# Kernel tuning notes

Hardware: AMD Instinct MI355X
Metric: run time of the kernel (lower is better)

Reference implementation:

```python
import jax, jax.numpy as jnp
import numpy as np

N_NODES = 100000

def setup_inputs() -> dict:
    key = jax.random.key(0)
    k1, k2, k3, k4, k5, k6 = jax.random.split(key, 6)
    input = jax.random.normal(k1, (N_NODES, 256), dtype=jnp.float32)
    weight = jax.random.normal(k2, (256, 256), dtype=jnp.float32) * (1.0 / np.sqrt(256))
    bias = jax.random.normal(k3, (256,), dtype=jnp.float32) * 0.02
    edge_rows = jax.random.randint(k4, (3200000,), 0, N_NODES, dtype=jnp.int32)
    edge_cols = jax.random.randint(k5, (3200000,), 0, N_NODES, dtype=jnp.int32)
    edge_vals = jax.random.uniform(k6, (3200000,), dtype=jnp.float32)
    return {"input": input, "weight": weight, "bias": bias,
            "edge_rows": edge_rows, "edge_cols": edge_cols, "edge_vals": edge_vals}

def reference(input, weight, bias, edge_rows, edge_cols, edge_vals):
    # support = X @ W  -- dense GEMM [N, in] x [in, out]
    support = input @ weight
    # output = spmm(adj, support): out[r] += adj[r,c] * support[c]
    gathered = support[edge_cols] * edge_vals[:, None]          # [E, out]
    output = jax.ops.segment_sum(gathered, edge_rows, num_segments=N_NODES)
    return output + bias
```

## Files before the change

kernel.cpp:

```cpp
#include <hip/hip_runtime.h>
#include <hip/hip_bf16.h>
#include <stdint.h>

#define M_NODES 100000
#define DIM     256
#define N_EDGES 3200000
#define CAP     80
#define CHUNK   8192
#define NWG1    391
#define NB      391
#define BCAP    9216

typedef __bf16 bf16x8 __attribute__((ext_vector_type(8)));
typedef float  f32x4  __attribute__((ext_vector_type(4)));
typedef unsigned short u16x8 __attribute__((ext_vector_type(8)));

__device__ __forceinline__ unsigned short f2bf(float f) {
    unsigned u = __float_as_uint(f);
    u += 0x7FFF + ((u >> 16) & 1);
    return (unsigned short)(u >> 16);
}
__device__ __forceinline__ float bf2f(unsigned short h) {
    return __uint_as_float(((unsigned)h) << 16);
}

__global__ __launch_bounds__(256) void k_convert_wt(const float* __restrict__ W,
                                                    unsigned short* __restrict__ Wt,
                                                    int* __restrict__ cur) {
    int k = blockIdx.x, n = threadIdx.x;
    Wt[n * 256 + k] = f2bf(W[k * 256 + n]);
    int gid = k * 256 + n;
    if (gid < NB) cur[gid] = 0;
}

__global__ __launch_bounds__(256) void k_gemm(const float* __restrict__ X,
                                              const unsigned short* __restrict__ Wt,
                                              unsigned short* __restrict__ Sb) {
    int wave = threadIdx.x >> 6;
    int lane = threadIdx.x & 63;
    int tile = blockIdx.x * 4 + wave;
    if (tile >= M_NODES / 16) return;
    int m0   = tile * 16;
    int quad = lane >> 4;
    int r    = lane & 15;

    const float* aptr = X + (size_t)(m0 + r) * 256 + quad * 8;

    f32x4 acc[16];
#pragma unroll
    for (int t = 0; t < 16; ++t) acc[t] = {0.f, 0.f, 0.f, 0.f};

#pragma unroll
    for (int k0 = 0; k0 < 256; k0 += 32) {
        f32x4 a0 = *(const f32x4*)(aptr + k0);
        f32x4 a1 = *(const f32x4*)(aptr + k0 + 4);
        unsigned short au[8];
        au[0] = f2bf(a0.x); au[1] = f2bf(a0.y); au[2] = f2bf(a0.z); au[3] = f2bf(a0.w);
        au[4] = f2bf(a1.x); au[5] = f2bf(a1.y); au[6] = f2bf(a1.z); au[7] = f2bf(a1.w);
        bf16x8 a = *(bf16x8*)au;
#pragma unroll
        for (int t = 0; t < 16; ++t) {
            bf16x8 b = *(const bf16x8*)(Wt + (size_t)(t * 16 + r) * 256 + k0 + quad * 8);
            acc[t] = __builtin_amdgcn_mfma_f32_16x16x32_bf16(a, b, acc[t], 0, 0, 0);
        }
    }

#pragma unroll
    for (int t = 0; t < 16; ++t)
#pragma unroll
        for (int i = 0; i < 4; ++i)
            Sb[(size_t)(m0 + quad * 4 + i) * 256 + t * 16 + r] = f2bf(acc[t][i]);
}

__global__ __launch_bounds__(512) void k_part2(const int* __restrict__ rows,
                                               const int* __restrict__ cols,
                                               const float* __restrict__ vals,
                                               uint64_t* __restrict__ part,
                                               int* __restrict__ cur) {
    __shared__ int cnt[NB];
    __shared__ int wcur[NB];
    int w = blockIdx.x, t = threadIdx.x;
    int base = w * CHUNK;
    int clen = N_EDGES - base; if (clen > CHUNK) clen = CHUNK;

    for (int i = t; i < NB; i += 512) cnt[i] = 0;
    __syncthreads();
    for (int i = t; i < clen; i += 512)
        atomicAdd(&cnt[rows[base + i] >> 8], 1);
    __syncthreads();

    for (int b = t; b < NB; b += 512)
        wcur[b] = atomicAdd(&cur[b], cnt[b]);
    __syncthreads();

    for (int i = t; i < clen; i += 512) {
        int   r = rows[base + i];
        int   c = cols[base + i];
        float v = vals[base + i];
        int   b = r >> 8;
        int pos = atomicAdd(&wcur[b], 1);
        if (pos < BCAP) {
            uint32_t lo = (uint32_t)c | ((uint32_t)(r & 255) << 17);
            part[(size_t)b * BCAP + pos] = ((uint64_t)__float_as_uint(v) << 32) | lo;
        }
    }
}

__global__ __launch_bounds__(512) void k_build3(const uint64_t* __restrict__ part,
                                                const int* __restrict__ cur,
                                                uint32_t* __restrict__ csr4,
                                                int* __restrict__ counts) {
    __shared__ int lcnt[256];
    int b = blockIdx.x, t = threadIdx.x;
    if (t < 256) lcnt[t] = 0;
    int n = cur[b];
    if (n > BCAP) n = BCAP;
    __syncthreads();

    const uint64_t* p = part + (size_t)b * BCAP;
    for (int i = t; i < n; i += 512) {
        uint64_t ent = p[i];
        uint32_t lo  = (uint32_t)ent;
        int   rl = (lo >> 17) & 255;
        int   c  = lo & 0x1FFFF;
        float v  = __uint_as_float((uint32_t)(ent >> 32));
        int qv = (int)(v * 32768.f + 0.5f);
        if (qv > 32767) qv = 32767;
        int pos = atomicAdd(&lcnt[rl], 1);
        if (pos < CAP)
            csr4[(size_t)(b * 256 + rl) * CAP + pos] = ((uint32_t)c << 15) | (uint32_t)qv;
    }
    __syncthreads();
    if (t < 256) counts[b * 256 + t] = lcnt[t];
}

__global__ __launch_bounds__(256) void k_spmm(const int* __restrict__ counts,
                                              const uint32_t* __restrict__ csr4,
                                              const unsigned short* __restrict__ Sb,
                                              const float* __restrict__ bias,
                                              float* __restrict__ out) {
    int wave = threadIdx.x >> 6;
    int lane = threadIdx.x & 63;
    int r = blockIdx.x * 4 + wave;
    if (r >= M_NODES) return;
    int n = counts[r];
    if (n > CAP) n = CAP;
    const uint32_t* ep = csr4 + (size_t)r * CAP;
    int half = lane >> 5;
    int l    = lane & 31;

    float acc[8] = {0.f, 0.f, 0.f, 0.f, 0.f, 0.f, 0.f, 0.f};
    int j = 0;
    for (; j + 7 < n; j += 8) {
        uint32_t m0 = ep[j +     half];
        uint32_t m1 = ep[j + 2 + half];
        uint32_t m2 = ep[j + 4 + half];
        uint32_t m3 = ep[j + 6 + half];
        int c0 = m0 >> 15;  float v0 = (float)(m0 & 0x7FFF) * (1.f / 32768.f);
        int c1 = m1 >> 15;  float v1 = (float)(m1 & 0x7FFF) * (1.f / 32768.f);
        int c2 = m2 >> 15;  float v2 = (float)(m2 & 0x7FFF) * (1.f / 32768.f);
        int c3 = m3 >> 15;  float v3 = (float)(m3 & 0x7FFF) * (1.f / 32768.f);
        u16x8 s0 = *(const u16x8*)(Sb + (size_t)c0 * 256 + l * 8);
        u16x8 s1 = *(const u16x8*)(Sb + (size_t)c1 * 256 + l * 8);
        u16x8 s2 = *(const u16x8*)(Sb + (size_t)c2 * 256 + l * 8);
        u16x8 s3 = *(const u16x8*)(Sb + (size_t)c3 * 256 + l * 8);
#pragma unroll
        for (int i = 0; i < 8; ++i) acc[i] += bf2f(s0[i]) * v0;
#pragma unroll
        for (int i = 0; i < 8; ++i) acc[i] += bf2f(s1[i]) * v1;
#pragma unroll
        for (int i = 0; i < 8; ++i) acc[i] += bf2f(s2[i]) * v2;
#pragma unroll
        for (int i = 0; i < 8; ++i) acc[i] += bf2f(s3[i]) * v3;
    }
    for (; j + 1 < n; j += 2) {
        uint32_t m0 = ep[j + half];
        int c0 = m0 >> 15;  float v0 = (float)(m0 & 0x7FFF) * (1.f / 32768.f);
        u16x8 s0 = *(const u16x8*)(Sb + (size_t)c0 * 256 + l * 8);
#pragma unroll
        for (int i = 0; i < 8; ++i) acc[i] += bf2f(s0[i]) * v0;
    }
    if (j < n && half == 0) {
        uint32_t m0 = ep[j];
        int c0 = m0 >> 15;  float v0 = (float)(m0 & 0x7FFF) * (1.f / 32768.f);
        u16x8 s0 = *(const u16x8*)(Sb + (size_t)c0 * 256 + l * 8);
#pragma unroll
        for (int i = 0; i < 8; ++i) acc[i] += bf2f(s0[i]) * v0;
    }

#pragma unroll
    for (int i = 0; i < 8; ++i) acc[i] += __shfl(acc[i], lane + 32);

    if (half == 0) {
        f32x4 b0 = *(const f32x4*)(bias + l * 8);
        f32x4 b1 = *(const f32x4*)(bias + l * 8 + 4);
        f32x4 o0 = {acc[0] + b0.x, acc[1] + b0.y, acc[2] + b0.z, acc[3] + b0.w};
        f32x4 o1 = {acc[4] + b1.x, acc[5] + b1.y, acc[6] + b1.z, acc[7] + b1.w};
        float* op = out + (size_t)r * 256 + l * 8;
        *(f32x4*)op       = o0;
        *(f32x4*)(op + 4) = o1;
    }
}

extern "C" void kernel_launch(void* const* d_in, const int* in_sizes, int n_in,
                              void* d_out, int out_size, void* d_ws, size_t ws_size,
                              hipStream_t stream) {
    const float* X    = (const float*)d_in[0];
    const float* W    = (const float*)d_in[1];
    const float* bias = (const float*)d_in[2];
    const int*   er   = (const int*)d_in[3];
    const int*   ec   = (const int*)d_in[4];
    const float* ev   = (const float*)d_in[5];
    float* out = (float*)d_out;

    char* ws = (char*)d_ws;
    unsigned short* Wt     = (unsigned short*)ws;
    uint32_t*       csr4   = (uint32_t*)(ws + 131072);
    int*            cur    = (int*)(ws + 32161792);
    int*            counts = (int*)(ws + 32166912);
    uint64_t*       part   = (uint64_t*)(ws + 32567296);
    unsigned short* Sb     = (unsigned short*)(ws + 32567296);

    k_convert_wt<<<256,   256, 0, stream>>>(W, Wt, cur);
    k_part2     <<<NWG1,  512, 0, stream>>>(er, ec, ev, part, cur);
    k_build3    <<<NB,    512, 0, stream>>>(part, cur, csr4, counts);
    k_gemm      <<<1563,  256, 0, stream>>>(X, Wt, Sb);
    k_spmm      <<<25000, 256, 0, stream>>>(counts, csr4, Sb, bias, out);
}
```

Measured before the change: 615.0 us.

## Fuse GEMM and edge partitioning into one kernel with interleaved block roles

The dense GEMM and the edge bucketing pass now run in a single launch: even blocks compute a GEMM tile and odd blocks partition a smaller edge chunk. This lets the compute-bound GEMM overlap with the memory- and atomic-bound partition step and drops one launch. Because the two now run at the same time, Sb moves to its own workspace region instead of aliasing part. The build kernel goes to 1024 threads per block, and empty buckets skip their global atomic. Smaller chunks mean more global atomics on the bucket cursors, and the mixed block roles may unbalance the workload.

```diff
diff --git a/kernel.cpp b/kernel.cpp
--- a/kernel.cpp
+++ b/kernel.cpp
@@ -6,8 +6,8 @@
 #define DIM     256
 #define N_EDGES 3200000
 #define CAP     80
-#define CHUNK   8192
-#define NWG1    391
+#define CHUNK   2048
+#define NCHUNK  1563
 #define NB      391
 #define BCAP    9216
 
@@ -33,67 +33,72 @@
     if (gid < NB) cur[gid] = 0;
 }
 
-__global__ __launch_bounds__(256) void k_gemm(const float* __restrict__ X,
-                                              const unsigned short* __restrict__ Wt,
-                                              unsigned short* __restrict__ Sb) {
-    int wave = threadIdx.x >> 6;
-    int lane = threadIdx.x & 63;
-    int tile = blockIdx.x * 4 + wave;
-    if (tile >= M_NODES / 16) return;
-    int m0   = tile * 16;
-    int quad = lane >> 4;
-    int r    = lane & 15;
-
-    const float* aptr = X + (size_t)(m0 + r) * 256 + quad * 8;
-
-    f32x4 acc[16];
-#pragma unroll
-    for (int t = 0; t < 16; ++t) acc[t] = {0.f, 0.f, 0.f, 0.f};
-
-#pragma unroll
-    for (int k0 = 0; k0 < 256; k0 += 32) {
-        f32x4 a0 = *(const f32x4*)(aptr + k0);
-        f32x4 a1 = *(const f32x4*)(aptr + k0 + 4);
-        unsigned short au[8];
-        au[0] = f2bf(a0.x); au[1] = f2bf(a0.y); au[2] = f2bf(a0.z); au[3] = f2bf(a0.w);
-        au[4] = f2bf(a1.x); au[5] = f2bf(a1.y); au[6] = f2bf(a1.z); au[7] = f2bf(a1.w);
-        bf16x8 a = *(bf16x8*)au;
-#pragma unroll
-        for (int t = 0; t < 16; ++t) {
-            bf16x8 b = *(const bf16x8*)(Wt + (size_t)(t * 16 + r) * 256 + k0 + quad * 8);
-            acc[t] = __builtin_amdgcn_mfma_f32_16x16x32_bf16(a, b, acc[t], 0, 0, 0);
-        }
-    }
-
-#pragma unroll
-    for (int t = 0; t < 16; ++t)
-#pragma unroll
-        for (int i = 0; i < 4; ++i)
-            Sb[(size_t)(m0 + quad * 4 + i) * 256 + t * 16 + r] = f2bf(acc[t][i]);
-}
-
-__global__ __launch_bounds__(512) void k_part2(const int* __restrict__ rows,
+__global__ __launch_bounds__(256) void k_fused(const float* __restrict__ X,
+                                               const unsigned short* __restrict__ Wt,
+                                               unsigned short* __restrict__ Sb,
+                                               const int* __restrict__ rows,
                                                const int* __restrict__ cols,
                                                const float* __restrict__ vals,
                                                uint64_t* __restrict__ part,
                                                int* __restrict__ cur) {
     __shared__ int cnt[NB];
     __shared__ int wcur[NB];
-    int w = blockIdx.x, t = threadIdx.x;
+    int bid = blockIdx.x;
+    int t   = threadIdx.x;
+
+    if ((bid & 1) == 0) {
+        int wave = t >> 6;
+        int lane = t & 63;
+        int tile = (bid >> 1) * 4 + wave;
+        if (tile >= M_NODES / 16) return;
+        int m0   = tile * 16;
+        int quad = lane >> 4;
+        int r    = lane & 15;
+
+        const float* aptr = X + (size_t)(m0 + r) * 256 + quad * 8;
+
+        f32x4 acc[16];
+#pragma unroll
+        for (int tt = 0; tt < 16; ++tt) acc[tt] = {0.f, 0.f, 0.f, 0.f};
+
+#pragma unroll
+        for (int k0 = 0; k0 < 256; k0 += 32) {
+            f32x4 a0 = *(const f32x4*)(aptr + k0);
+            f32x4 a1 = *(const f32x4*)(aptr + k0 + 4);
+            unsigned short au[8];
+            au[0] = f2bf(a0.x); au[1] = f2bf(a0.y); au[2] = f2bf(a0.z); au[3] = f2bf(a0.w);
+            au[4] = f2bf(a1.x); au[5] = f2bf(a1.y); au[6] = f2bf(a1.z); au[7] = f2bf(a1.w);
+            bf16x8 a = *(bf16x8*)au;
+#pragma unroll
+            for (int tt = 0; tt < 16; ++tt) {
+                bf16x8 b = *(const bf16x8*)(Wt + (size_t)(tt * 16 + r) * 256 + k0 + quad * 8);
+                acc[tt] = __builtin_amdgcn_mfma_f32_16x16x32_bf16(a, b, acc[tt], 0, 0, 0);
+            }
+        }
+
+#pragma unroll
+        for (int tt = 0; tt < 16; ++tt)
+#pragma unroll
+            for (int i = 0; i < 4; ++i)
+                Sb[(size_t)(m0 + quad * 4 + i) * 256 + tt * 16 + r] = f2bf(acc[tt][i]);
+        return;
+    }
+
+    int w    = bid >> 1;
     int base = w * CHUNK;
     int clen = N_EDGES - base; if (clen > CHUNK) clen = CHUNK;
 
-    for (int i = t; i < NB; i += 512) cnt[i] = 0;
-    __syncthreads();
-    for (int i = t; i < clen; i += 512)
+    for (int i = t; i < NB; i += 256) cnt[i] = 0;
+    __syncthreads();
+    for (int i = t; i < clen; i += 256)
         atomicAdd(&cnt[rows[base + i] >> 8], 1);
     __syncthreads();
 
-    for (int b = t; b < NB; b += 512)
-        wcur[b] = atomicAdd(&cur[b], cnt[b]);
-    __syncthreads();
-
-    for (int i = t; i < clen; i += 512) {
+    for (int b = t; b < NB; b += 256)
+        if (cnt[b]) wcur[b] = atomicAdd(&cur[b], cnt[b]);
+    __syncthreads();
+
+    for (int i = t; i < clen; i += 256) {
         int   r = rows[base + i];
         int   c = cols[base + i];
         float v = vals[base + i];
@@ -106,10 +111,10 @@
     }
 }
 
-__global__ __launch_bounds__(512) void k_build3(const uint64_t* __restrict__ part,
-                                                const int* __restrict__ cur,
-                                                uint32_t* __restrict__ csr4,
-                                                int* __restrict__ counts) {
+__global__ __launch_bounds__(1024) void k_build3(const uint64_t* __restrict__ part,
+                                                 const int* __restrict__ cur,
+                                                 uint32_t* __restrict__ csr4,
+                                                 int* __restrict__ counts) {
     __shared__ int lcnt[256];
     int b = blockIdx.x, t = threadIdx.x;
     if (t < 256) lcnt[t] = 0;
@@ -118,7 +123,7 @@
     __syncthreads();
 
     const uint64_t* p = part + (size_t)b * BCAP;
-    for (int i = t; i < n; i += 512) {
+    for (int i = t; i < n; i += 1024) {
         uint64_t ent = p[i];
         uint32_t lo  = (uint32_t)ent;
         int   rl = (lo >> 17) & 255;
@@ -219,11 +224,10 @@
     int*            cur    = (int*)(ws + 32161792);
     int*            counts = (int*)(ws + 32166912);
     uint64_t*       part   = (uint64_t*)(ws + 32567296);
-    unsigned short* Sb     = (unsigned short*)(ws + 32567296);
-
-    k_convert_wt<<<256,   256, 0, stream>>>(W, Wt, cur);
-    k_part2     <<<NWG1,  512, 0, stream>>>(er, ec, ev, part, cur);
-    k_build3    <<<NB,    512, 0, stream>>>(part, cur, csr4, counts);
-    k_gemm      <<<1563,  256, 0, stream>>>(X, Wt, Sb);
-    k_spmm      <<<25000, 256, 0, stream>>>(counts, csr4, Sb, bias, out);
-}
+    unsigned short* Sb     = (unsigned short*)(ws + 61394944);
+
+    k_convert_wt<<<256,        256,  0, stream>>>(W, Wt, cur);
+    k_fused     <<<2 * NCHUNK, 256,  0, stream>>>(X, Wt, Sb, er, ec, ev, part, cur);
+    k_build3    <<<NB,         1024, 0, stream>>>(part, cur, csr4, counts);
+    k_spmm      <<<25000,      256,  0, stream>>>(counts, csr4, Sb, bias, out);
+}
```

Measured after the change: 658.0 us. 1.07x slower.
